# Optimization experiments

Measured on AMD Instinct MI355X. Metric: run time of the kernel, lower is better.

The kernel has to match this reference:

```python
import jax, jax.numpy as jnp
import numpy as np

B, S, DIN, DOUT = 4, 2048, 4096, 4096

def setup_inputs() -> dict:
    key = jax.random.key(0)
    k1, k2, k3 = jax.random.split(key, 3)
    inputs = jax.random.normal(k1, (B, S, DIN), dtype=jnp.float32)
    # int8 quantized weight stored as int8, simulated per-channel symmetric quant
    weight = jax.random.randint(k2, (DOUT, DIN), -127, 127, dtype=jnp.int32).astype(jnp.int8)
    weight_scaler = jax.random.uniform(k3, (DOUT,), dtype=jnp.float32) * 0.02
    return {"inputs": inputs, "weight": weight, "weight_scaler": weight_scaler}

def reference(inputs, weight, weight_scaler):
    # F.linear(inputs, weight) * weight_scaler
    # int8 weight is upcast for the matmul; per-output-channel dequant scale applied after.
    w = weight.astype(inputs.dtype)            # [DOUT, DIN]
    out = jnp.einsum('bsi,oi->bso', inputs, w) # [B, S, DOUT]
    return out * weight_scaler                 # broadcast over last dim
```

## Files before the change

kernel.cpp:

```cpp
#include <hip/hip_runtime.h>
#include <hip/hip_bf16.h>
#include <cstdint>

#define M_DIM 8192
#define N_DIM 4096
#define K_DIM 4096

typedef unsigned short u16;
typedef unsigned int u32;
typedef __attribute__((ext_vector_type(8))) short short8;
typedef __attribute__((ext_vector_type(4))) float floatx4;

#define AS1 __attribute__((address_space(1)))
#define AS3 __attribute__((address_space(3)))

static __device__ __forceinline__ u16 f2bf(float f) {
    u32 x = __float_as_uint(f);
    x += 0x7FFFu + ((x >> 16) & 1u);
    return (u16)(x >> 16);
}

__global__ void cvt_a_kernel(const float4* __restrict__ in, ushort4* __restrict__ out, int n4) {
    int i = blockIdx.x * blockDim.x + threadIdx.x;
    int stride = gridDim.x * blockDim.x;
    for (; i < n4; i += stride) {
        float4 f = in[i];
        ushort4 u;
        u.x = f2bf(f.x); u.y = f2bf(f.y); u.z = f2bf(f.z); u.w = f2bf(f.w);
        out[i] = u;
    }
}

__global__ void cvt_w_kernel(const int4* __restrict__ in, ushort4* __restrict__ out, int n4) {
    int i = blockIdx.x * blockDim.x + threadIdx.x;
    int stride = gridDim.x * blockDim.x;
    for (; i < n4; i += stride) {
        int4 w = in[i];
        ushort4 u;
        u.x = f2bf((float)w.x);
        u.y = f2bf((float)w.y);
        u.z = f2bf((float)w.z);
        u.w = f2bf((float)w.w);
        out[i] = u;
    }
}

__global__ void __launch_bounds__(256)
gemm_bf16_kernel(const u16* __restrict__ A, const u16* __restrict__ W,
                 const float* __restrict__ scaler, float* __restrict__ out) {
    __shared__ u16 As[128 * 32];
    __shared__ u16 Bs[128 * 32];

    const int tid  = threadIdx.x;
    const int wave = tid >> 6;
    const int lane = tid & 63;
    const int r = lane & 15;
    const int q = lane >> 4;

    const int mBase = blockIdx.y * 128;
    const int nBase = blockIdx.x * 128;
    const int waveM = wave >> 1;
    const int waveN = wave & 1;

    floatx4 acc[4][4] = {};

    const int rowA  = tid >> 2;
    const int swzW  = (rowA >> 1) & 3;
    const int chunk = (tid & 3) ^ swzW;
    const u16* aSrc0 = A + (size_t)(mBase + rowA) * K_DIM + chunk * 8;
    const u16* aSrc1 = A + (size_t)(mBase + 64 + rowA) * K_DIM + chunk * 8;
    const u16* bSrc0 = W + (size_t)(nBase + rowA) * K_DIM + chunk * 8;
    const u16* bSrc1 = W + (size_t)(nBase + 64 + rowA) * K_DIM + chunk * 8;
    char* aDst0 = (char*)As + wave * 1024;
    char* aDst1 = (char*)As + 4096 + wave * 1024;
    char* bDst0 = (char*)Bs + wave * 1024;
    char* bDst1 = (char*)Bs + 4096 + wave * 1024;

    const int swzR = (r >> 1) & 3;
    const u16* aRead = As + (waveM * 64 + r) * 32 + (q ^ swzR) * 8;
    const u16* bRead = Bs + (waveN * 64 + r) * 32 + (q ^ swzR) * 8;

    for (int kt = 0; kt < K_DIM / 32; ++kt) {
        const int kOff = kt * 32;
        __builtin_amdgcn_global_load_lds((const AS1 u32*)(const void*)(aSrc0 + kOff),
                                         (AS3 u32*)(void*)aDst0, 16, 0, 0);
        __builtin_amdgcn_global_load_lds((const AS1 u32*)(const void*)(aSrc1 + kOff),
                                         (AS3 u32*)(void*)aDst1, 16, 0, 0);
        __builtin_amdgcn_global_load_lds((const AS1 u32*)(const void*)(bSrc0 + kOff),
                                         (AS3 u32*)(void*)bDst0, 16, 0, 0);
        __builtin_amdgcn_global_load_lds((const AS1 u32*)(const void*)(bSrc1 + kOff),
                                         (AS3 u32*)(void*)bDst1, 16, 0, 0);
        __syncthreads();

        short8 a[4], b[4];
#pragma unroll
        for (int mt = 0; mt < 4; ++mt) a[mt] = *(const short8*)(aRead + mt * 16 * 32);
#pragma unroll
        for (int nt = 0; nt < 4; ++nt) b[nt] = *(const short8*)(bRead + nt * 16 * 32);
#pragma unroll
        for (int mt = 0; mt < 4; ++mt)
#pragma unroll
            for (int nt = 0; nt < 4; ++nt)
                acc[mt][nt] = __builtin_amdgcn_mfma_f32_16x16x32_bf16(a[mt], b[nt], acc[mt][nt], 0, 0, 0);

        __syncthreads();
    }

    const int mW = mBase + waveM * 64;
    const int nW = nBase + waveN * 64;
#pragma unroll
    for (int nt = 0; nt < 4; ++nt) {
        const int n = nW + nt * 16 + r;
        const float s = scaler[n];
#pragma unroll
        for (int mt = 0; mt < 4; ++mt) {
            const int m0 = mW + mt * 16 + q * 4;
#pragma unroll
            for (int j = 0; j < 4; ++j)
                out[(size_t)(m0 + j) * N_DIM + n] = acc[mt][nt][j] * s;
        }
    }
}

__global__ void __launch_bounds__(256)
gemm_fallback_kernel(const float* __restrict__ A, const int* __restrict__ W,
                     const float* __restrict__ scaler, float* __restrict__ out) {
    __shared__ float As[64][33];
    __shared__ float Ws[64][33];
    const int tx = threadIdx.x & 15, ty = threadIdx.x >> 4;
    const int mBase = blockIdx.y * 64, nBase = blockIdx.x * 64;
    float acc[4][4] = {};
    for (int kt = 0; kt < K_DIM; kt += 32) {
        for (int i = threadIdx.x; i < 64 * 32; i += 256) {
            int rr = i >> 5, cc = i & 31;
            As[rr][cc] = A[(size_t)(mBase + rr) * K_DIM + kt + cc];
            Ws[rr][cc] = (float)W[(size_t)(nBase + rr) * K_DIM + kt + cc];
        }
        __syncthreads();
        for (int kk = 0; kk < 32; ++kk) {
            float av[4], bv[4];
#pragma unroll
            for (int i = 0; i < 4; ++i) av[i] = As[ty * 4 + i][kk];
#pragma unroll
            for (int j = 0; j < 4; ++j) bv[j] = Ws[tx * 4 + j][kk];
#pragma unroll
            for (int i = 0; i < 4; ++i)
#pragma unroll
                for (int j = 0; j < 4; ++j) acc[i][j] += av[i] * bv[j];
        }
        __syncthreads();
    }
#pragma unroll
    for (int i = 0; i < 4; ++i)
#pragma unroll
        for (int j = 0; j < 4; ++j) {
            int m = mBase + ty * 4 + i, n = nBase + tx * 4 + j;
            out[(size_t)m * N_DIM + n] = acc[i][j] * scaler[n];
        }
}

extern "C" void kernel_launch(void* const* d_in, const int* in_sizes, int n_in,
                              void* d_out, int out_size, void* d_ws, size_t ws_size,
                              hipStream_t stream) {
    const float* A      = (const float*)d_in[0];
    const int*   W32    = (const int*)d_in[1];
    const float* scaler = (const float*)d_in[2];
    float* out          = (float*)d_out;

    const size_t needA = (size_t)M_DIM * K_DIM * sizeof(u16);
    const size_t needW = (size_t)N_DIM * K_DIM * sizeof(u16);

    if (ws_size >= needA + needW) {
        u16* Abf = (u16*)d_ws;
        u16* Wbf = (u16*)((char*)d_ws + needA);
        cvt_a_kernel<<<4096, 256, 0, stream>>>((const float4*)A, (ushort4*)Abf, M_DIM * K_DIM / 4);
        cvt_w_kernel<<<2048, 256, 0, stream>>>((const int4*)W32, (ushort4*)Wbf, N_DIM * K_DIM / 4);
        dim3 grid(N_DIM / 128, M_DIM / 128);
        gemm_bf16_kernel<<<grid, 256, 0, stream>>>(Abf, Wbf, scaler, out);
    } else {
        dim3 grid(N_DIM / 64, M_DIM / 64);
        gemm_fallback_kernel<<<grid, 256, 0, stream>>>(A, W32, scaler, out);
    }
}
```

Measured before the change: 573.6 us.

## Replace bf16 GEMM with 256x256 double-buffered, phase-pipelined MFMA kernel

Replaces the 128x128 single-buffered GEMM with a 256x256 tile kernel using 8 waves, K-step 64, and a double-buffered LDS pipeline that prefetches two K-tiles ahead via global_load_lds. Each K-tile is split into four phases that interleave LDS fragment reads and async stage issues with MFMA bursts, using raw barriers, explicit vmcnt/lgkmcnt waits and s_setprio. The goal is to raise arithmetic intensity and hide global-memory latency behind compute. In exchange it uses the full 128KB of LDS and many more accumulator registers, and its correctness depends on hand-tuned wait counts.

```diff
diff --git a/kernel.cpp b/kernel.cpp
--- a/kernel.cpp
+++ b/kernel.cpp
@@ -1,5 +1,4 @@
 #include <hip/hip_runtime.h>
-#include <hip/hip_bf16.h>
 #include <cstdint>
 
 #define M_DIM 8192
@@ -45,77 +44,152 @@
     }
 }
 
-__global__ void __launch_bounds__(256)
-gemm_bf16_kernel(const u16* __restrict__ A, const u16* __restrict__ W,
-                 const float* __restrict__ scaler, float* __restrict__ out) {
-    __shared__ u16 As[128 * 32];
-    __shared__ u16 Bs[128 * 32];
+
+#define GLL(s, d) __builtin_amdgcn_global_load_lds((const AS1 u32*)(const void*)(s), \
+                                                   (AS3 u32*)(void*)(d), 16, 0, 0)
+
+#define STAGE_A(kt, h, d) do { \
+    const u16* s_ = aSrcTh + (size_t)(h) * (128 * K_DIM) + (size_t)(kt) * 64; \
+    char* d_ = ldsC + (d) * 65536 + (h) * 16384 + waveOff; \
+    GLL(s_, d_); \
+    GLL(s_ + 64 * K_DIM, d_ + 8192); \
+} while (0)
+
+#define STAGE_B(kt, h, d) do { \
+    const u16* s_ = bSrcTh + (size_t)(h) * (128 * K_DIM) + (size_t)(kt) * 64; \
+    char* d_ = ldsC + 32768 + (d) * 65536 + (h) * 16384 + waveOff; \
+    GLL(s_, d_); \
+    GLL(s_ + 64 * K_DIM, d_ + 8192); \
+} while (0)
+
+#define RD(off) (*(const short8*)&lds[(off)])
+#define MMA(d, a, b) (d) = __builtin_amdgcn_mfma_f32_16x16x32_bf16((a), (b), (d), 0, 0, 0)
+#define BAR() __builtin_amdgcn_s_barrier()
+#define FENCE() asm volatile("" ::: "memory")
+#define WAIT_LGKM0() asm volatile("s_waitcnt lgkmcnt(0)" ::: "memory")
+
+#define PH0(bt) do { \
+    _Pragma("unroll") for (int mt_ = 0; mt_ < 4; ++mt_) { \
+      aF[mt_][0] = RD((bt) * 32768 + aRowOff + mt_ * 1024 + c0); \
+      aF[mt_][1] = RD((bt) * 32768 + aRowOff + mt_ * 1024 + c1); \
+    } \
+    _Pragma("unroll") for (int nt_ = 0; nt_ < 2; ++nt_) { \
+      bF0[nt_][0] = RD((bt) * 32768 + 16384 + bRowOff + nt_ * 1024 + c0); \
+      bF0[nt_][1] = RD((bt) * 32768 + 16384 + bRowOff + nt_ * 1024 + c1); \
+    } \
+    BAR(); WAIT_LGKM0(); \
+    __builtin_amdgcn_s_setprio(1); \
+    _Pragma("unroll") for (int mt_ = 0; mt_ < 4; ++mt_) \
+      _Pragma("unroll") for (int nt_ = 0; nt_ < 2; ++nt_) { \
+        MMA(acc[mt_][nt_], aF[mt_][0], bF0[nt_][0]); \
+        MMA(acc[mt_][nt_], aF[mt_][1], bF0[nt_][1]); \
+      } \
+    __builtin_amdgcn_s_setprio(0); \
+    BAR(); FENCE(); \
+} while (0)
+
+#define PH1(bt) do { \
+    _Pragma("unroll") for (int nt_ = 0; nt_ < 2; ++nt_) { \
+      bF1[nt_][0] = RD((bt) * 32768 + 16384 + bRowOff + (2 + nt_) * 1024 + c0); \
+      bF1[nt_][1] = RD((bt) * 32768 + 16384 + bRowOff + (2 + nt_) * 1024 + c1); \
+    } \
+    BAR(); WAIT_LGKM0(); \
+    __builtin_amdgcn_s_setprio(1); \
+    _Pragma("unroll") for (int mt_ = 0; mt_ < 4; ++mt_) \
+      _Pragma("unroll") for (int nt_ = 0; nt_ < 2; ++nt_) { \
+        MMA(acc[mt_][2 + nt_], aF[mt_][0], bF1[nt_][0]); \
+        MMA(acc[mt_][2 + nt_], aF[mt_][1], bF1[nt_][1]); \
+      } \
+    __builtin_amdgcn_s_setprio(0); \
+    BAR(); FENCE(); \
+} while (0)
+
+#define PH2(t, bt, doStg) do { \
+    _Pragma("unroll") for (int mt_ = 0; mt_ < 4; ++mt_) { \
+      aF[mt_][0] = RD((bt) * 32768 + aRowOff + (4 + mt_) * 1024 + c0); \
+      aF[mt_][1] = RD((bt) * 32768 + aRowOff + (4 + mt_) * 1024 + c1); \
+    } \
+    if (doStg) { STAGE_B((t) + 2, 0, (bt)); STAGE_B((t) + 2, 1, (bt)); } \
+    BAR(); WAIT_LGKM0(); \
+    __builtin_amdgcn_s_setprio(1); \
+    _Pragma("unroll") for (int mt_ = 0; mt_ < 4; ++mt_) \
+      _Pragma("unroll") for (int nt_ = 0; nt_ < 2; ++nt_) { \
+        MMA(acc[4 + mt_][nt_], aF[mt_][0], bF0[nt_][0]); \
+        MMA(acc[4 + mt_][nt_], aF[mt_][1], bF0[nt_][1]); \
+      } \
+    __builtin_amdgcn_s_setprio(0); \
+    BAR(); FENCE(); \
+} while (0)
+
+#define PH3(t, bt, doStg, VM) do { \
+    if (doStg) { STAGE_A((t) + 2, 0, (bt)); STAGE_A((t) + 2, 1, (bt)); } \
+    asm volatile("s_waitcnt vmcnt(" #VM ")" ::: "memory"); \
+    BAR(); WAIT_LGKM0(); \
+    __builtin_amdgcn_s_setprio(1); \
+    _Pragma("unroll") for (int mt_ = 0; mt_ < 4; ++mt_) \
+      _Pragma("unroll") for (int nt_ = 0; nt_ < 2; ++nt_) { \
+        MMA(acc[4 + mt_][2 + nt_], aF[mt_][0], bF1[nt_][0]); \
+        MMA(acc[4 + mt_][2 + nt_], aF[mt_][1], bF1[nt_][1]); \
+      } \
+    __builtin_amdgcn_s_setprio(0); \
+    BAR(); FENCE(); \
+} while (0)
+
+__global__ void __launch_bounds__(512, 2)
+gemm_bf16_256(const u16* __restrict__ A, const u16* __restrict__ W,
+              const float* __restrict__ scaler, float* __restrict__ out) {
+    __shared__ u16 lds[65536];
 
     const int tid  = threadIdx.x;
     const int wave = tid >> 6;
     const int lane = tid & 63;
     const int r = lane & 15;
     const int q = lane >> 4;
-
-    const int mBase = blockIdx.y * 128;
-    const int nBase = blockIdx.x * 128;
-    const int waveM = wave >> 1;
-    const int waveN = wave & 1;
-
-    floatx4 acc[4][4] = {};
-
-    const int rowA  = tid >> 2;
-    const int swzW  = (rowA >> 1) & 3;
-    const int chunk = (tid & 3) ^ swzW;
-    const u16* aSrc0 = A + (size_t)(mBase + rowA) * K_DIM + chunk * 8;
-    const u16* aSrc1 = A + (size_t)(mBase + 64 + rowA) * K_DIM + chunk * 8;
-    const u16* bSrc0 = W + (size_t)(nBase + rowA) * K_DIM + chunk * 8;
-    const u16* bSrc1 = W + (size_t)(nBase + 64 + rowA) * K_DIM + chunk * 8;
-    char* aDst0 = (char*)As + wave * 1024;
-    char* aDst1 = (char*)As + 4096 + wave * 1024;
-    char* bDst0 = (char*)Bs + wave * 1024;
-    char* bDst1 = (char*)Bs + 4096 + wave * 1024;
-
-    const int swzR = (r >> 1) & 3;
-    const u16* aRead = As + (waveM * 64 + r) * 32 + (q ^ swzR) * 8;
-    const u16* bRead = Bs + (waveN * 64 + r) * 32 + (q ^ swzR) * 8;
-
-    for (int kt = 0; kt < K_DIM / 32; ++kt) {
-        const int kOff = kt * 32;
-        __builtin_amdgcn_global_load_lds((const AS1 u32*)(const void*)(aSrc0 + kOff),
-                                         (AS3 u32*)(void*)aDst0, 16, 0, 0);
-        __builtin_amdgcn_global_load_lds((const AS1 u32*)(const void*)(aSrc1 + kOff),
-                                         (AS3 u32*)(void*)aDst1, 16, 0, 0);
-        __builtin_amdgcn_global_load_lds((const AS1 u32*)(const void*)(bSrc0 + kOff),
-                                         (AS3 u32*)(void*)bDst0, 16, 0, 0);
-        __builtin_amdgcn_global_load_lds((const AS1 u32*)(const void*)(bSrc1 + kOff),
-                                         (AS3 u32*)(void*)bDst1, 16, 0, 0);
-        __syncthreads();
-
-        short8 a[4], b[4];
-#pragma unroll
-        for (int mt = 0; mt < 4; ++mt) a[mt] = *(const short8*)(aRead + mt * 16 * 32);
-#pragma unroll
-        for (int nt = 0; nt < 4; ++nt) b[nt] = *(const short8*)(bRead + nt * 16 * 32);
-#pragma unroll
-        for (int mt = 0; mt < 4; ++mt)
-#pragma unroll
-            for (int nt = 0; nt < 4; ++nt)
-                acc[mt][nt] = __builtin_amdgcn_mfma_f32_16x16x32_bf16(a[mt], b[nt], acc[mt][nt], 0, 0, 0);
-
-        __syncthreads();
-    }
-
-    const int mW = mBase + waveM * 64;
+    const int waveM = wave >> 2;
+    const int waveN = wave & 3;
+
+    const int mBase = blockIdx.y * 256;
+    const int nBase = blockIdx.x * 256;
+
+    const int aRowOff = (waveM * 128 + r) * 64;
+    const int bRowOff = (waveN * 64 + r) * 64;
+    const int c0 = (q ^ (r & 7)) * 8;
+    const int c1 = c0 ^ 32;
+    const int waveOff = wave * 1024;
+    char* ldsC = (char*)lds;
+
+    const int srow = tid >> 3;
+    const int schk = (tid & 7) ^ (srow & 7);
+    const u16* aSrcTh = A + (size_t)(mBase + srow) * K_DIM + schk * 8;
+    const u16* bSrcTh = W + (size_t)(nBase + srow) * K_DIM + schk * 8;
+
+    short8 aF[4][2], bF0[2][2], bF1[2][2];
+    floatx4 acc[8][4] = {};
+
+    STAGE_B(0, 0, 0); STAGE_B(0, 1, 0); STAGE_A(0, 0, 0); STAGE_A(0, 1, 0);
+    STAGE_B(1, 0, 1); STAGE_B(1, 1, 1); STAGE_A(1, 0, 1); STAGE_A(1, 1, 1);
+    asm volatile("s_waitcnt vmcnt(8)" ::: "memory");
+    BAR(); FENCE();
+
+    #pragma unroll 1
+    for (int tt = 0; tt < 31; ++tt) {
+        const int t0 = 2 * tt;
+        PH0(0); PH1(0); PH2(t0, 0, 1); PH3(t0, 0, 1, 8);
+        PH0(1); PH1(1); PH2(t0 + 1, 1, 1); PH3(t0 + 1, 1, 1, 8);
+    }
+    PH0(0); PH1(0); PH2(62, 0, 0); PH3(62, 0, 0, 0);
+    PH0(1); PH1(1); PH2(63, 1, 0); PH3(63, 1, 0, 0);
+
+    const int mW = mBase + waveM * 128;
     const int nW = nBase + waveN * 64;
-#pragma unroll
+    #pragma unroll
     for (int nt = 0; nt < 4; ++nt) {
         const int n = nW + nt * 16 + r;
         const float s = scaler[n];
-#pragma unroll
-        for (int mt = 0; mt < 4; ++mt) {
+        #pragma unroll
+        for (int mt = 0; mt < 8; ++mt) {
             const int m0 = mW + mt * 16 + q * 4;
-#pragma unroll
+            #pragma unroll
             for (int j = 0; j < 4; ++j)
                 out[(size_t)(m0 + j) * N_DIM + n] = acc[mt][nt][j] * s;
         }
@@ -175,8 +249,8 @@
         u16* Wbf = (u16*)((char*)d_ws + needA);
         cvt_a_kernel<<<4096, 256, 0, stream>>>((const float4*)A, (ushort4*)Abf, M_DIM * K_DIM / 4);
         cvt_w_kernel<<<2048, 256, 0, stream>>>((const int4*)W32, (ushort4*)Wbf, N_DIM * K_DIM / 4);
-        dim3 grid(N_DIM / 128, M_DIM / 128);
-        gemm_bf16_kernel<<<grid, 256, 0, stream>>>(Abf, Wbf, scaler, out);
+        dim3 grid(N_DIM / 256, M_DIM / 256);
+        gemm_bf16_256<<<grid, 512, 0, stream>>>(Abf, Wbf, scaler, out);
     } else {
         dim3 grid(N_DIM / 64, M_DIM / 64);
         gemm_fallback_kernel<<<grid, 256, 0, stream>>>(A, W32, scaler, out);
```

New measurement: 483.3 us. 15.7% less time.
